# Kernel optimization log

Measured on AMD Instinct MI355X. Metric: run time of the kernel, lower is better.

## Reference

```python
import jax, jax.numpy as jnp
import numpy as np

E = 16        # num_experts
TOPK = 2      # num_experts_per_tok


def setup_inputs() -> dict:
    key = jax.random.key(0)
    ks = jax.random.split(key, 8)
    B, S, H, I, IS = 4, 2048, 1024, 512, 2048
    std = 0.02
    return {
        "hidden_states": jax.random.normal(ks[0], (B, S, H), jnp.float32),
        "gate_w": jax.random.normal(ks[1], (E, H), jnp.float32) * std,
        "gate_up_proj": jax.random.normal(ks[2], (E, 2 * I, H), jnp.float32) * std,
        "down_proj": jax.random.normal(ks[3], (E, H, I), jnp.float32) * std,
        "shared_gate_proj": jax.random.normal(ks[4], (IS, H), jnp.float32) * std,
        "shared_up_proj": jax.random.normal(ks[5], (IS, H), jnp.float32) * std,
        "shared_down_proj": jax.random.normal(ks[6], (H, IS), jnp.float32) * std,
        "shared_expert_gate_w": jax.random.normal(ks[7], (1, H), jnp.float32) * std,
    }


def _moe(x, gate_w, gate_up_proj, down_proj, sgp, sup, sdp, segw):
    # x: [N, H] flattened tokens
    N = x.shape[0]
    router_logits = x @ gate_w.T                      # [N, E]
    probs = jax.nn.softmax(router_logits, axis=-1)
    routing_weights, selected = jax.lax.top_k(probs, TOPK)   # [N, TOPK]
    routing_weights = routing_weights / routing_weights.sum(-1, keepdims=True)
    # combine weights scattered into dense [N, E] (per-token per-expert gate)
    combine = jnp.zeros((N, E), x.dtype).at[jnp.arange(N)[:, None], selected].add(routing_weights)

    def body(acc, ws):
        gu_w, d_w, cw = ws                            # [2I,H], [H,I], [N]
        gu = x @ gu_w.T                               # [N, 2I]
        g, u = jnp.split(gu, 2, axis=-1)
        h = jax.nn.silu(g) * u                        # [N, I]
        return acc + cw[:, None] * (h @ d_w.T), None

    expert_out, _ = jax.lax.scan(body, jnp.zeros_like(x), (gate_up_proj, down_proj, combine.T))

    # shared expert with sigmoid token gate
    shared_h = jax.nn.silu(x @ sgp.T) * (x @ sup.T)   # [N, IS]
    shared_out = (shared_h @ sdp.T) * jax.nn.sigmoid(x @ segw.T)  # [N, H]
    out = expert_out + shared_out

    # aux (load-balancing) loss
    counts = jnp.sum(jax.nn.one_hot(selected, E, dtype=x.dtype), axis=(0, 1))  # [E]
    frac_tokens = counts / (N * TOPK)
    frac_probs = probs.sum(0) / N
    aux_loss = E * jnp.sum(frac_tokens * frac_probs)
    return out, aux_loss


def reference(hidden_states, gate_w, gate_up_proj, down_proj, shared_gate_proj, shared_up_proj, shared_down_proj, shared_expert_gate_w):
    B, S, H = hidden_states.shape
    out, aux = _moe(hidden_states.reshape(-1, H), gate_w, gate_up_proj, down_proj,
                    shared_gate_proj, shared_up_proj, shared_down_proj, shared_expert_gate_w)
    return out.reshape(B, S, H), aux
```

## Files before the change

kernel.cpp:

```cpp
#include <hip/hip_runtime.h>
#include <hip/hip_bf16.h>
#include <stdint.h>


#define N_TOK 8192
#define HDIM 1024
#define NEXP 16
#define IEXP 512
#define ISH 2048

typedef __bf16 bf16x8 __attribute__((ext_vector_type(8)));
typedef float f32x4 __attribute__((ext_vector_type(4)));

#define OFF_XBF   ((size_t)0)
#define OFF_WSG   ((size_t)16777216)
#define OFF_WSU   ((size_t)20971520)
#define OFF_WSD   ((size_t)25165824)
#define OFF_SH    ((size_t)29360128)
#define OFF_HEXP  ((size_t)62914560)
#define OFF_IDS   ((size_t)79691776)
#define OFF_META  ((size_t)80216064)
#define OFF_SIG   ((size_t)80216320)
#define OFF_LG    ((size_t)80249088)
#define OFF_SLOT  ((size_t)81297664)
#define OFF_TWAB  ((size_t)81363200)

static __device__ __forceinline__ unsigned short f2bf(float f) {
  unsigned int u = __float_as_uint(f);
  u += 0x7fffu + ((u >> 16) & 1u);
  return (unsigned short)(u >> 16);
}
static __device__ __forceinline__ int pack_bf2(float a, float b) {
  return (int)f2bf(a) | ((int)f2bf(b) << 16);
}
static __device__ __forceinline__ float bf2f(unsigned short u) {
  return __uint_as_float(((unsigned int)u) << 16);
}
static __device__ __forceinline__ void gl_lds16(const void* g, void* l) {
  __builtin_amdgcn_global_load_lds(
      (const __attribute__((address_space(1))) unsigned int*)g,
      (__attribute__((address_space(3))) unsigned int*)l, 16, 0, 0);
}

__global__ void cvt_kernel(const float* __restrict__ src,
                           unsigned short* __restrict__ dst, int n4) {
  int i = blockIdx.x * 256 + threadIdx.x;
  if (i >= n4) return;
  float4 v = ((const float4*)src)[i];
  uint2 o;
  o.x = (unsigned)pack_bf2(v.x, v.y);
  o.y = (unsigned)pack_bf2(v.z, v.w);
  ((uint2*)dst)[i] = o;
}

__global__ __launch_bounds__(256) void logits_kernel(
    const float* __restrict__ X, const float* __restrict__ GW,
    const float* __restrict__ SEGW, float* __restrict__ LG,
    unsigned short* __restrict__ XBF) {
  int wid = threadIdx.x >> 6, lane = threadIdx.x & 63;
  int tok = blockIdx.x * 4 + wid;
  const float* xr = X + (size_t)tok * HDIM;
  unsigned short* xw = XBF + (size_t)tok * HDIM;
  float xv[16];
#pragma unroll
  for (int i = 0; i < 16; i++) xv[i] = xr[lane + 64 * i];
#pragma unroll
  for (int i = 0; i < 16; i++) xw[lane + 64 * i] = f2bf(xv[i]);
  float myv = 0.f;
#pragma unroll
  for (int e = 0; e < 17; e++) {
    const float* wr = (e < 16) ? (GW + (size_t)e * HDIM) : SEGW;
    float p = 0.f;
#pragma unroll
    for (int i = 0; i < 16; i++) p += xv[i] * wr[lane + 64 * i];
#pragma unroll
    for (int off = 32; off >= 1; off >>= 1) p += __shfl_xor(p, off, 64);
    if (lane == e) myv = p;
  }
  if (lane < 17) LG[(size_t)tok * 32 + lane] = myv;
}

__global__ __launch_bounds__(256) void route_kernel(
    const float* __restrict__ LG, int* __restrict__ cnt,
    float* __restrict__ pps, int* __restrict__ ids,
    int* __restrict__ slotAB, float* __restrict__ twAB,
    float* __restrict__ sig) {
  __shared__ int lcnt[16];
  __shared__ int lbase[16];
  __shared__ float lps[16];
  int tid = threadIdx.x;
  int tok = blockIdx.x * 256 + tid;
  if (tid < 16) { lcnt[tid] = 0; lps[tid] = 0.f; }
  __syncthreads();
  const float4* row = (const float4*)(LG + (size_t)tok * 32);
  float4 v0 = row[0], v1 = row[1], v2 = row[2], v3 = row[3];
  float g16 = row[4].x;
  float lg[16] = {v0.x, v0.y, v0.z, v0.w, v1.x, v1.y, v1.z, v1.w,
                  v2.x, v2.y, v2.z, v2.w, v3.x, v3.y, v3.z, v3.w};
  float mx = lg[0];
#pragma unroll
  for (int e = 1; e < 16; e++) mx = fmaxf(mx, lg[e]);
  float pr[16], s = 0.f;
#pragma unroll
  for (int e = 0; e < 16; e++) { pr[e] = __expf(lg[e] - mx); s += pr[e]; }
  float inv_s = 1.f / s;
  float p1 = -1.f, p2 = -1.f; int i1 = 0, i2 = 0;
#pragma unroll
  for (int e = 0; e < 16; e++) {
    if (pr[e] > p1) { p2 = p1; i2 = i1; p1 = pr[e]; i1 = e; }
    else if (pr[e] > p2) { p2 = pr[e]; i2 = e; }
  }
  float wsum = p1 + p2;
  int s1 = atomicAdd(&lcnt[i1], 1);
  int s2 = atomicAdd(&lcnt[i2], 1);
#pragma unroll
  for (int e = 0; e < 16; e++) atomicAdd(&lps[e], pr[e] * inv_s);
  sig[tok] = 1.f / (1.f + __expf(-g16));
  __syncthreads();
  if (tid < 16) {
    lbase[tid] = atomicAdd(&cnt[tid], lcnt[tid]);
    atomicAdd(&pps[tid], lps[tid]);
  }
  __syncthreads();
  int sl1 = lbase[i1] + s1, sl2 = lbase[i2] + s2;
  ids[i1 * N_TOK + sl1] = tok;
  ids[i2 * N_TOK + sl2] = tok;
  slotAB[tok * 2]     = (i1 << 14) | sl1;
  slotAB[tok * 2 + 1] = (i2 << 14) | sl2;
  twAB[tok * 2]     = p1 / wsum;
  twAB[tok * 2 + 1] = p2 / wsum;
}

__global__ void offs_aux_kernel(const int* __restrict__ cnt, int* __restrict__ off,
                                const float* __restrict__ probs_sum,
                                float* __restrict__ out_aux) {
  if (threadIdx.x == 0 && blockIdx.x == 0) {
    int run = 0; float aux = 0.f;
    for (int e = 0; e < NEXP; e++) {
      off[e] = run; run += cnt[e];
      aux += ((float)cnt[e] / (float)(N_TOK * 2)) * (probs_sum[e] / (float)N_TOK);
    }
    off[16] = run;
    *out_aux = (float)NEXP * aux;
  }
}

__global__ __launch_bounds__(256) void shared_gemm1_kernel(
    const unsigned short* __restrict__ X, const unsigned short* __restrict__ Wg,
    const unsigned short* __restrict__ Wu, unsigned short* __restrict__ H) {
  __shared__ __align__(16) unsigned short As[128 * 32];
  __shared__ __align__(16) unsigned short Bs1[64 * 32];
  __shared__ __align__(16) unsigned short Bs2[64 * 32];
  int m0 = blockIdx.y * 128, n0 = blockIdx.x * 64;
  int t = threadIdx.x, lane = t & 63, w = t >> 6;
  int wm = (w & 1) * 64, wn = (w >> 1) * 32;
  int arow = t >> 2, akb = (t & 3) * 8;
  const unsigned short* ap0 = X + (size_t)(m0 + arow) * HDIM + akb;
  const unsigned short* ap1 = X + (size_t)(m0 + 64 + arow) * HDIM + akb;
  const unsigned short* bp1 = Wg + (size_t)(n0 + arow) * HDIM + akb;
  const unsigned short* bp2 = Wu + (size_t)(n0 + arow) * HDIM + akb;
  f32x4 z = {0.f, 0.f, 0.f, 0.f};
  f32x4 accg[4][2], accu[4][2];
#pragma unroll
  for (int i = 0; i < 4; i++)
#pragma unroll
    for (int j = 0; j < 2; j++) { accg[i][j] = z; accu[i][j] = z; }
  for (int k0 = 0; k0 < HDIM; k0 += 32) {
    __syncthreads();
    gl_lds16(ap0 + k0, &As[t * 8]);
    gl_lds16(ap1 + k0, &As[2048 + t * 8]);
    gl_lds16(bp1 + k0, &Bs1[t * 8]);
    gl_lds16(bp2 + k0, &Bs2[t * 8]);
    __syncthreads();
    int fr = lane & 15, fc = (lane >> 4) * 8;
    bf16x8 af[4], bg[2], bu[2];
#pragma unroll
    for (int i = 0; i < 4; i++) af[i] = *(const bf16x8*)&As[(wm + i * 16 + fr) * 32 + fc];
#pragma unroll
    for (int j = 0; j < 2; j++) {
      bg[j] = *(const bf16x8*)&Bs1[(wn + j * 16 + fr) * 32 + fc];
      bu[j] = *(const bf16x8*)&Bs2[(wn + j * 16 + fr) * 32 + fc];
    }
#pragma unroll
    for (int i = 0; i < 4; i++)
#pragma unroll
      for (int j = 0; j < 2; j++) {
        accg[i][j] = __builtin_amdgcn_mfma_f32_16x16x32_bf16(af[i], bg[j], accg[i][j], 0, 0, 0);
        accu[i][j] = __builtin_amdgcn_mfma_f32_16x16x32_bf16(af[i], bu[j], accu[i][j], 0, 0, 0);
      }
  }
  int col = lane & 15, rq = (lane >> 4) * 4;
#pragma unroll
  for (int i = 0; i < 4; i++)
#pragma unroll
    for (int j = 0; j < 2; j++)
#pragma unroll
      for (int r = 0; r < 4; r++) {
        int mm = m0 + wm + i * 16 + rq + r;
        int nn = n0 + wn + j * 16 + col;
        float g = accg[i][j][r], u = accu[i][j][r];
        float h = g / (1.f + __expf(-g)) * u;
        H[(size_t)mm * ISH + nn] = f2bf(h);
      }
}

__global__ __launch_bounds__(256) void shared_gemm2_kernel(
    const unsigned short* __restrict__ H, const unsigned short* __restrict__ Wd,
    const float* __restrict__ sig, float* __restrict__ Out) {
  __shared__ __align__(16) unsigned short As[128 * 32];
  __shared__ __align__(16) unsigned short Bs[128 * 32];
  int m0 = blockIdx.y * 128, n0 = blockIdx.x * 128;
  int t = threadIdx.x, lane = t & 63, w = t >> 6;
  int wm = (w & 1) * 64, wn = (w >> 1) * 64;
  int arow = t >> 2, akb = (t & 3) * 8;
  const unsigned short* apA0 = H + (size_t)(m0 + arow) * ISH + akb;
  const unsigned short* apA1 = H + (size_t)(m0 + 64 + arow) * ISH + akb;
  const unsigned short* apB0 = Wd + (size_t)(n0 + arow) * ISH + akb;
  const unsigned short* apB1 = Wd + (size_t)(n0 + 64 + arow) * ISH + akb;
  f32x4 z = {0.f, 0.f, 0.f, 0.f};
  f32x4 acc[4][4];
#pragma unroll
  for (int i = 0; i < 4; i++)
#pragma unroll
    for (int j = 0; j < 4; j++) acc[i][j] = z;
  for (int k0 = 0; k0 < ISH; k0 += 32) {
    __syncthreads();
    gl_lds16(apA0 + k0, &As[t * 8]);
    gl_lds16(apA1 + k0, &As[2048 + t * 8]);
    gl_lds16(apB0 + k0, &Bs[t * 8]);
    gl_lds16(apB1 + k0, &Bs[2048 + t * 8]);
    __syncthreads();
    int fr = lane & 15, fc = (lane >> 4) * 8;
    bf16x8 af[4], bfr[4];
#pragma unroll
    for (int i = 0; i < 4; i++) {
      af[i] = *(const bf16x8*)&As[(wm + i * 16 + fr) * 32 + fc];
      bfr[i] = *(const bf16x8*)&Bs[(wn + i * 16 + fr) * 32 + fc];
    }
#pragma unroll
    for (int i = 0; i < 4; i++)
#pragma unroll
      for (int j = 0; j < 4; j++)
        acc[i][j] = __builtin_amdgcn_mfma_f32_16x16x32_bf16(af[i], bfr[j], acc[i][j], 0, 0, 0);
  }
  int col = lane & 15, rq = (lane >> 4) * 4;
#pragma unroll
  for (int i = 0; i < 4; i++)
#pragma unroll
    for (int r = 0; r < 4; r++) {
      int mm = m0 + wm + i * 16 + rq + r;
      float sg = sig[mm];
#pragma unroll
      for (int j = 0; j < 4; j++) {
        int nn = n0 + wn + j * 16 + col;
        Out[(size_t)mm * HDIM + nn] = acc[i][j][r] * sg;
      }
    }
}

__global__ __launch_bounds__(256) void exp_gemm1_kernel(
    const unsigned short* __restrict__ X, const unsigned short* __restrict__ WGUb,
    const int* __restrict__ ids, const int* __restrict__ cnt,
    const int* __restrict__ off, unsigned short* __restrict__ Hexp) {
  int e = blockIdx.z;
  int ne = cnt[e];
  int m0 = blockIdx.y * 128;
  if (m0 >= ne) return;
  __shared__ __align__(16) unsigned short As[128 * 32];
  __shared__ __align__(16) unsigned short Bs1[64 * 32];
  __shared__ __align__(16) unsigned short Bs2[64 * 32];
  int n0 = blockIdx.x * 64;
  const int* eids = ids + e * N_TOK;
  int base = off[e];
  int t = threadIdx.x, lane = t & 63, w = t >> 6;
  int wm = (w & 1) * 64, wn = (w >> 1) * 32;
  int arow = t >> 2, akb = (t & 3) * 8;
  int s0 = m0 + arow, s1 = m0 + 64 + arow;
  int t0 = (s0 < ne) ? eids[s0] : 0;
  int t1 = (s1 < ne) ? eids[s1] : 0;
  const unsigned short* ap0 = X + (size_t)t0 * HDIM + akb;
  const unsigned short* ap1 = X + (size_t)t1 * HDIM + akb;
  const unsigned short* bpg = WGUb + ((size_t)e * 1024 + n0 + arow) * HDIM + akb;
  const unsigned short* bpu = WGUb + ((size_t)e * 1024 + 512 + n0 + arow) * HDIM + akb;
  f32x4 z = {0.f, 0.f, 0.f, 0.f};
  f32x4 accg[4][2], accu[4][2];
#pragma unroll
  for (int i = 0; i < 4; i++)
#pragma unroll
    for (int j = 0; j < 2; j++) { accg[i][j] = z; accu[i][j] = z; }
  for (int k0 = 0; k0 < HDIM; k0 += 32) {
    __syncthreads();
    gl_lds16(ap0 + k0, &As[t * 8]);
    gl_lds16(ap1 + k0, &As[2048 + t * 8]);
    gl_lds16(bpg + k0, &Bs1[t * 8]);
    gl_lds16(bpu + k0, &Bs2[t * 8]);
    __syncthreads();
    int fr = lane & 15, fc = (lane >> 4) * 8;
    bf16x8 af[4], bg[2], bu[2];
#pragma unroll
    for (int i = 0; i < 4; i++) af[i] = *(const bf16x8*)&As[(wm + i * 16 + fr) * 32 + fc];
#pragma unroll
    for (int j = 0; j < 2; j++) {
      bg[j] = *(const bf16x8*)&Bs1[(wn + j * 16 + fr) * 32 + fc];
      bu[j] = *(const bf16x8*)&Bs2[(wn + j * 16 + fr) * 32 + fc];
    }
#pragma unroll
    for (int i = 0; i < 4; i++)
#pragma unroll
      for (int j = 0; j < 2; j++) {
        accg[i][j] = __builtin_amdgcn_mfma_f32_16x16x32_bf16(af[i], bg[j], accg[i][j], 0, 0, 0);
        accu[i][j] = __builtin_amdgcn_mfma_f32_16x16x32_bf16(af[i], bu[j], accu[i][j], 0, 0, 0);
      }
  }
  int col = lane & 15, rq = (lane >> 4) * 4;
#pragma unroll
  for (int i = 0; i < 4; i++)
#pragma unroll
    for (int j = 0; j < 2; j++)
#pragma unroll
      for (int r = 0; r < 4; r++) {
        int slot = m0 + wm + i * 16 + rq + r;
        if (slot < ne) {
          int nn = n0 + wn + j * 16 + col;
          float g = accg[i][j][r], u = accu[i][j][r];
          float h = g / (1.f + __expf(-g)) * u;
          Hexp[(size_t)(base + slot) * IEXP + nn] = f2bf(h);
        }
      }
}

__global__ __launch_bounds__(256) void exp_gemm2_kernel(
    const unsigned short* __restrict__ Hexp, const unsigned short* __restrict__ WDb,
    const int* __restrict__ cnt, const int* __restrict__ off,
    unsigned short* __restrict__ Eout) {
  int e = blockIdx.z;
  int ne = cnt[e];
  int m0 = blockIdx.y * 128;
  if (m0 >= ne) return;
  __shared__ __align__(16) unsigned short As[128 * 32];
  __shared__ __align__(16) unsigned short Bs[128 * 32];
  int n0 = blockIdx.x * 128;
  int base = off[e];
  int t = threadIdx.x, lane = t & 63, w = t >> 6;
  int wm = (w & 1) * 64, wn = (w >> 1) * 64;
  int arow = t >> 2, akb = (t & 3) * 8;
  int ra0 = base + m0 + arow;        if (ra0 > 16383) ra0 = 16383;
  int ra1 = base + m0 + 64 + arow;   if (ra1 > 16383) ra1 = 16383;
  const unsigned short* ap0 = Hexp + (size_t)ra0 * IEXP + akb;
  const unsigned short* ap1 = Hexp + (size_t)ra1 * IEXP + akb;
  const unsigned short* bp0 = WDb + ((size_t)e * HDIM + n0 + arow) * IEXP + akb;
  const unsigned short* bp1 = WDb + ((size_t)e * HDIM + n0 + 64 + arow) * IEXP + akb;
  f32x4 z = {0.f, 0.f, 0.f, 0.f};
  f32x4 acc[4][4];
#pragma unroll
  for (int i = 0; i < 4; i++)
#pragma unroll
    for (int j = 0; j < 4; j++) acc[i][j] = z;
  for (int k0 = 0; k0 < IEXP; k0 += 32) {
    __syncthreads();
    gl_lds16(ap0 + k0, &As[t * 8]);
    gl_lds16(ap1 + k0, &As[2048 + t * 8]);
    gl_lds16(bp0 + k0, &Bs[t * 8]);
    gl_lds16(bp1 + k0, &Bs[2048 + t * 8]);
    __syncthreads();
    int fr = lane & 15, fc = (lane >> 4) * 8;
    bf16x8 af[4], bfr[4];
#pragma unroll
    for (int i = 0; i < 4; i++) {
      af[i] = *(const bf16x8*)&As[(wm + i * 16 + fr) * 32 + fc];
      bfr[i] = *(const bf16x8*)&Bs[(wn + i * 16 + fr) * 32 + fc];
    }
#pragma unroll
    for (int i = 0; i < 4; i++)
#pragma unroll
      for (int j = 0; j < 4; j++)
        acc[i][j] = __builtin_amdgcn_mfma_f32_16x16x32_bf16(af[i], bfr[j], acc[i][j], 0, 0, 0);
  }
  int col = lane & 15, rq = (lane >> 4) * 4;
#pragma unroll
  for (int i = 0; i < 4; i++)
#pragma unroll
    for (int r = 0; r < 4; r++) {
      int slot = m0 + wm + i * 16 + rq + r;
      if (slot < ne) {
#pragma unroll
        for (int j = 0; j < 4; j++) {
          int nn = n0 + wn + j * 16 + col;
          Eout[(size_t)(base + slot) * HDIM + nn] = f2bf(acc[i][j][r]);
        }
      }
    }
}

__global__ __launch_bounds__(256) void combine_kernel(
    const unsigned short* __restrict__ Eout, const int* __restrict__ slotAB,
    const float* __restrict__ twAB, const int* __restrict__ off,
    float* __restrict__ Out) {
  int tok = blockIdx.x, t = threadIdx.x;
  int sa = slotAB[tok * 2], sb = slotAB[tok * 2 + 1];
  float wa = twAB[tok * 2], wb = twAB[tok * 2 + 1];
  int ra = off[sa >> 14] + (sa & 16383);
  int rb = off[sb >> 14] + (sb & 16383);
  const ushort4 a4 = *(const ushort4*)(Eout + (size_t)ra * HDIM + t * 4);
  const ushort4 b4 = *(const ushort4*)(Eout + (size_t)rb * HDIM + t * 4);
  float* po = Out + (size_t)tok * HDIM + t * 4;
  float4 o = *(const float4*)po;
  o.x += wa * bf2f(a4.x) + wb * bf2f(b4.x);
  o.y += wa * bf2f(a4.y) + wb * bf2f(b4.y);
  o.z += wa * bf2f(a4.z) + wb * bf2f(b4.z);
  o.w += wa * bf2f(a4.w) + wb * bf2f(b4.w);
  *(float4*)po = o;
}

extern "C" void kernel_launch(void* const* d_in, const int* in_sizes, int n_in,
                              void* d_out, int out_size, void* d_ws, size_t ws_size,
                              hipStream_t stream) {
  const float* X   = (const float*)d_in[0];
  const float* GW  = (const float*)d_in[1];
  const float* WGU = (const float*)d_in[2];
  const float* WDN = (const float*)d_in[3];
  const float* WSG = (const float*)d_in[4];
  const float* WSU = (const float*)d_in[5];
  const float* WSD = (const float*)d_in[6];
  const float* SEGW = (const float*)d_in[7];
  float* Out = (float*)d_out;
  char* ws = (char*)d_ws;

  unsigned short* xbf  = (unsigned short*)(ws + OFF_XBF);
  unsigned short* wsg  = (unsigned short*)(ws + OFF_WSG);
  unsigned short* wsu  = (unsigned short*)(ws + OFF_WSU);
  unsigned short* wsd  = (unsigned short*)(ws + OFF_WSD);
  unsigned short* sh   = (unsigned short*)(ws + OFF_SH);
  unsigned short* hexp = (unsigned short*)(ws + OFF_HEXP);
  int*   ids  = (int*)(ws + OFF_IDS);
  int*   cnt  = (int*)(ws + OFF_META);
  int*   off  = (int*)(ws + OFF_META + 64);
  float* pps  = (float*)(ws + OFF_META + 144);
  float* sig  = (float*)(ws + OFF_SIG);
  float* lg   = (float*)(ws + OFF_LG);
  int*   slotAB = (int*)(ws + OFF_SLOT);
  float* twAB   = (float*)(ws + OFF_TWAB);
  unsigned short* wgu_bf = (unsigned short*)(ws + OFF_SH);
  unsigned short* wdn_bf = (unsigned short*)(ws + OFF_XBF);
  unsigned short* eout   = (unsigned short*)(ws + OFF_SH);

  hipMemsetAsync(ws + OFF_META, 0, 256, stream);

  {
    int n4;
    n4 = (ISH * HDIM) / 4;
    cvt_kernel<<<(n4 + 255) / 256, 256, 0, stream>>>(WSG, wsg, n4);
    cvt_kernel<<<(n4 + 255) / 256, 256, 0, stream>>>(WSU, wsu, n4);
    n4 = (HDIM * ISH) / 4;
    cvt_kernel<<<(n4 + 255) / 256, 256, 0, stream>>>(WSD, wsd, n4);
  }

  logits_kernel<<<N_TOK / 4, 256, 0, stream>>>(X, GW, SEGW, lg, xbf);
  route_kernel<<<N_TOK / 256, 256, 0, stream>>>(lg, cnt, pps, ids, slotAB, twAB, sig);
  offs_aux_kernel<<<1, 64, 0, stream>>>(cnt, off, pps, Out + (size_t)N_TOK * HDIM);

  shared_gemm1_kernel<<<dim3(ISH / 64, N_TOK / 128), 256, 0, stream>>>(xbf, wsg, wsu, sh);
  shared_gemm2_kernel<<<dim3(HDIM / 128, N_TOK / 128), 256, 0, stream>>>(sh, wsd, sig, Out);

  {
    int n4 = (NEXP * 2 * IEXP * HDIM) / 4;
    cvt_kernel<<<(n4 + 255) / 256, 256, 0, stream>>>(WGU, wgu_bf, n4);
  }
  exp_gemm1_kernel<<<dim3(IEXP / 64, N_TOK / 128, NEXP), 256, 0, stream>>>(
      xbf, wgu_bf, ids, cnt, off, hexp);
  {
    int n4 = (NEXP * HDIM * IEXP) / 4;
    cvt_kernel<<<(n4 + 255) / 256, 256, 0, stream>>>(WDN, wdn_bf, n4);
  }
  exp_gemm2_kernel<<<dim3(HDIM / 128, N_TOK / 128, NEXP), 256, 0, stream>>>(
      hexp, wdn_bf, cnt, off, eout);
  combine_kernel<<<N_TOK, 256, 0, stream>>>(eout, slotAB, twAB, off, Out);
}
```

Measured before the change: 491.5 us.

## Use BK=64 XOR-swizzled LDS tiles and batch weight conversions into one launch

All four GEMM kernels now stage K-tiles of 64 instead of 32 into LDS, with an XOR swizzle on the column offset. This halves the number of barrier pairs per K loop and is meant to avoid LDS bank conflicts on the fragment reads. shared_gemm2 moves to 64-wide N tiles, which doubles its grid. When the workspace is large enough, the five weight fp32-to-bf16 conversions are fused into a single cvt5 launch into separate buffers, removing four launches. The larger LDS footprint per block may lower occupancy.

```diff
diff --git a/kernel.cpp b/kernel.cpp
--- a/kernel.cpp
+++ b/kernel.cpp
@@ -24,6 +24,9 @@
 #define OFF_LG    ((size_t)80249088)
 #define OFF_SLOT  ((size_t)81297664)
 #define OFF_TWAB  ((size_t)81363200)
+#define OFF_WGU2  ((size_t)81428736)
+#define OFF_WDN2  ((size_t)114983168)
+#define WS_NEED_ROOMY ((size_t)131760384)
 
 static __device__ __forceinline__ unsigned short f2bf(float f) {
   unsigned int u = __float_as_uint(f);
@@ -51,6 +54,30 @@
   o.x = (unsigned)pack_bf2(v.x, v.y);
   o.y = (unsigned)pack_bf2(v.z, v.w);
   ((uint2*)dst)[i] = o;
+}
+
+__global__ void cvt5_kernel(const float* s0, unsigned short* d0, int c0,
+                            const float* s1, unsigned short* d1, int c1,
+                            const float* s2, unsigned short* d2, int c2,
+                            const float* s3, unsigned short* d3, int c3,
+                            const float* s4, unsigned short* d4, int c4) {
+  int i = blockIdx.x * 256 + threadIdx.x;
+  const float* s; unsigned short* d;
+  if (i < c0) { s = s0; d = d0; }
+  else { i -= c0;
+  if (i < c1) { s = s1; d = d1; }
+  else { i -= c1;
+  if (i < c2) { s = s2; d = d2; }
+  else { i -= c2;
+  if (i < c3) { s = s3; d = d3; }
+  else { i -= c3;
+  if (i < c4) { s = s4; d = d4; }
+  else return; }}}}
+  float4 v = ((const float4*)s)[i];
+  uint2 o;
+  o.x = (unsigned)pack_bf2(v.x, v.y);
+  o.y = (unsigned)pack_bf2(v.z, v.w);
+  ((uint2*)d)[i] = o;
 }
 
 __global__ __launch_bounds__(256) void logits_kernel(
@@ -145,49 +172,65 @@
   }
 }
 
+
 __global__ __launch_bounds__(256) void shared_gemm1_kernel(
     const unsigned short* __restrict__ X, const unsigned short* __restrict__ Wg,
     const unsigned short* __restrict__ Wu, unsigned short* __restrict__ H) {
-  __shared__ __align__(16) unsigned short As[128 * 32];
-  __shared__ __align__(16) unsigned short Bs1[64 * 32];
-  __shared__ __align__(16) unsigned short Bs2[64 * 32];
+  __shared__ __align__(16) unsigned short As[128 * 64];
+  __shared__ __align__(16) unsigned short Bs1[64 * 64];
+  __shared__ __align__(16) unsigned short Bs2[64 * 64];
   int m0 = blockIdx.y * 128, n0 = blockIdx.x * 64;
   int t = threadIdx.x, lane = t & 63, w = t >> 6;
   int wm = (w & 1) * 64, wn = (w >> 1) * 32;
-  int arow = t >> 2, akb = (t & 3) * 8;
-  const unsigned short* ap0 = X + (size_t)(m0 + arow) * HDIM + akb;
-  const unsigned short* ap1 = X + (size_t)(m0 + 64 + arow) * HDIM + akb;
-  const unsigned short* bp1 = Wg + (size_t)(n0 + arow) * HDIM + akb;
-  const unsigned short* bp2 = Wu + (size_t)(n0 + arow) * HDIM + akb;
+  int srow = t >> 3;
+  int scol = (((t & 7) ^ (srow & 7)) * 8);
+  const unsigned short* apA[4];
+#pragma unroll
+  for (int r = 0; r < 4; r++) apA[r] = X + (size_t)(m0 + r * 32 + srow) * HDIM + scol;
+  const unsigned short* apB1[2];
+  const unsigned short* apB2[2];
+#pragma unroll
+  for (int r = 0; r < 2; r++) {
+    apB1[r] = Wg + (size_t)(n0 + r * 32 + srow) * HDIM + scol;
+    apB2[r] = Wu + (size_t)(n0 + r * 32 + srow) * HDIM + scol;
+  }
+  int fr = lane & 15, q = lane >> 4, sw = fr & 7;
+  int fo0 = ((q ^ sw) * 8), fo1 = (((4 + q) ^ sw) * 8);
   f32x4 z = {0.f, 0.f, 0.f, 0.f};
   f32x4 accg[4][2], accu[4][2];
 #pragma unroll
   for (int i = 0; i < 4; i++)
 #pragma unroll
     for (int j = 0; j < 2; j++) { accg[i][j] = z; accu[i][j] = z; }
-  for (int k0 = 0; k0 < HDIM; k0 += 32) {
-    __syncthreads();
-    gl_lds16(ap0 + k0, &As[t * 8]);
-    gl_lds16(ap1 + k0, &As[2048 + t * 8]);
-    gl_lds16(bp1 + k0, &Bs1[t * 8]);
-    gl_lds16(bp2 + k0, &Bs2[t * 8]);
-    __syncthreads();
-    int fr = lane & 15, fc = (lane >> 4) * 8;
-    bf16x8 af[4], bg[2], bu[2];
-#pragma unroll
-    for (int i = 0; i < 4; i++) af[i] = *(const bf16x8*)&As[(wm + i * 16 + fr) * 32 + fc];
-#pragma unroll
-    for (int j = 0; j < 2; j++) {
-      bg[j] = *(const bf16x8*)&Bs1[(wn + j * 16 + fr) * 32 + fc];
-      bu[j] = *(const bf16x8*)&Bs2[(wn + j * 16 + fr) * 32 + fc];
-    }
-#pragma unroll
-    for (int i = 0; i < 4; i++)
+  for (int k0 = 0; k0 < HDIM; k0 += 64) {
+    __syncthreads();
+#pragma unroll
+    for (int r = 0; r < 4; r++) gl_lds16(apA[r] + k0, &As[r * 2048 + t * 8]);
+#pragma unroll
+    for (int r = 0; r < 2; r++) {
+      gl_lds16(apB1[r] + k0, &Bs1[r * 2048 + t * 8]);
+      gl_lds16(apB2[r] + k0, &Bs2[r * 2048 + t * 8]);
+    }
+    __syncthreads();
+#pragma unroll
+    for (int kk = 0; kk < 2; kk++) {
+      int fo = kk ? fo1 : fo0;
+      bf16x8 af[4], bg[2], bu[2];
+#pragma unroll
+      for (int i = 0; i < 4; i++) af[i] = *(const bf16x8*)&As[(wm + i * 16 + fr) * 64 + fo];
 #pragma unroll
       for (int j = 0; j < 2; j++) {
-        accg[i][j] = __builtin_amdgcn_mfma_f32_16x16x32_bf16(af[i], bg[j], accg[i][j], 0, 0, 0);
-        accu[i][j] = __builtin_amdgcn_mfma_f32_16x16x32_bf16(af[i], bu[j], accu[i][j], 0, 0, 0);
-      }
+        bg[j] = *(const bf16x8*)&Bs1[(wn + j * 16 + fr) * 64 + fo];
+        bu[j] = *(const bf16x8*)&Bs2[(wn + j * 16 + fr) * 64 + fo];
+      }
+#pragma unroll
+      for (int i = 0; i < 4; i++)
+#pragma unroll
+        for (int j = 0; j < 2; j++) {
+          accg[i][j] = __builtin_amdgcn_mfma_f32_16x16x32_bf16(af[i], bg[j], accg[i][j], 0, 0, 0);
+          accu[i][j] = __builtin_amdgcn_mfma_f32_16x16x32_bf16(af[i], bu[j], accu[i][j], 0, 0, 0);
+        }
+    }
   }
   int col = lane & 15, rq = (lane >> 4) * 4;
 #pragma unroll
@@ -207,41 +250,48 @@
 __global__ __launch_bounds__(256) void shared_gemm2_kernel(
     const unsigned short* __restrict__ H, const unsigned short* __restrict__ Wd,
     const float* __restrict__ sig, float* __restrict__ Out) {
-  __shared__ __align__(16) unsigned short As[128 * 32];
-  __shared__ __align__(16) unsigned short Bs[128 * 32];
-  int m0 = blockIdx.y * 128, n0 = blockIdx.x * 128;
+  __shared__ __align__(16) unsigned short As[128 * 64];
+  __shared__ __align__(16) unsigned short Bs[64 * 64];
+  int m0 = blockIdx.y * 128, n0 = blockIdx.x * 64;
   int t = threadIdx.x, lane = t & 63, w = t >> 6;
-  int wm = (w & 1) * 64, wn = (w >> 1) * 64;
-  int arow = t >> 2, akb = (t & 3) * 8;
-  const unsigned short* apA0 = H + (size_t)(m0 + arow) * ISH + akb;
-  const unsigned short* apA1 = H + (size_t)(m0 + 64 + arow) * ISH + akb;
-  const unsigned short* apB0 = Wd + (size_t)(n0 + arow) * ISH + akb;
-  const unsigned short* apB1 = Wd + (size_t)(n0 + 64 + arow) * ISH + akb;
+  int wm = (w & 1) * 64, wn = (w >> 1) * 32;
+  int srow = t >> 3;
+  int scol = (((t & 7) ^ (srow & 7)) * 8);
+  const unsigned short* apA[4];
+#pragma unroll
+  for (int r = 0; r < 4; r++) apA[r] = H + (size_t)(m0 + r * 32 + srow) * ISH + scol;
+  const unsigned short* apB[2];
+#pragma unroll
+  for (int r = 0; r < 2; r++) apB[r] = Wd + (size_t)(n0 + r * 32 + srow) * ISH + scol;
+  int fr = lane & 15, q = lane >> 4, sw = fr & 7;
+  int fo0 = ((q ^ sw) * 8), fo1 = (((4 + q) ^ sw) * 8);
   f32x4 z = {0.f, 0.f, 0.f, 0.f};
-  f32x4 acc[4][4];
-#pragma unroll
-  for (int i = 0; i < 4; i++)
-#pragma unroll
-    for (int j = 0; j < 4; j++) acc[i][j] = z;
-  for (int k0 = 0; k0 < ISH; k0 += 32) {
-    __syncthreads();
-    gl_lds16(apA0 + k0, &As[t * 8]);
-    gl_lds16(apA1 + k0, &As[2048 + t * 8]);
-    gl_lds16(apB0 + k0, &Bs[t * 8]);
-    gl_lds16(apB1 + k0, &Bs[2048 + t * 8]);
-    __syncthreads();
-    int fr = lane & 15, fc = (lane >> 4) * 8;
-    bf16x8 af[4], bfr[4];
-#pragma unroll
-    for (int i = 0; i < 4; i++) {
-      af[i] = *(const bf16x8*)&As[(wm + i * 16 + fr) * 32 + fc];
-      bfr[i] = *(const bf16x8*)&Bs[(wn + i * 16 + fr) * 32 + fc];
-    }
-#pragma unroll
-    for (int i = 0; i < 4; i++)
-#pragma unroll
-      for (int j = 0; j < 4; j++)
-        acc[i][j] = __builtin_amdgcn_mfma_f32_16x16x32_bf16(af[i], bfr[j], acc[i][j], 0, 0, 0);
+  f32x4 acc[4][2];
+#pragma unroll
+  for (int i = 0; i < 4; i++)
+#pragma unroll
+    for (int j = 0; j < 2; j++) acc[i][j] = z;
+  for (int k0 = 0; k0 < ISH; k0 += 64) {
+    __syncthreads();
+#pragma unroll
+    for (int r = 0; r < 4; r++) gl_lds16(apA[r] + k0, &As[r * 2048 + t * 8]);
+#pragma unroll
+    for (int r = 0; r < 2; r++) gl_lds16(apB[r] + k0, &Bs[r * 2048 + t * 8]);
+    __syncthreads();
+#pragma unroll
+    for (int kk = 0; kk < 2; kk++) {
+      int fo = kk ? fo1 : fo0;
+      bf16x8 af[4], bfr[2];
+#pragma unroll
+      for (int i = 0; i < 4; i++) af[i] = *(const bf16x8*)&As[(wm + i * 16 + fr) * 64 + fo];
+#pragma unroll
+      for (int j = 0; j < 2; j++) bfr[j] = *(const bf16x8*)&Bs[(wn + j * 16 + fr) * 64 + fo];
+#pragma unroll
+      for (int i = 0; i < 4; i++)
+#pragma unroll
+        for (int j = 0; j < 2; j++)
+          acc[i][j] = __builtin_amdgcn_mfma_f32_16x16x32_bf16(af[i], bfr[j], acc[i][j], 0, 0, 0);
+    }
   }
   int col = lane & 15, rq = (lane >> 4) * 4;
 #pragma unroll
@@ -251,7 +301,7 @@
       int mm = m0 + wm + i * 16 + rq + r;
       float sg = sig[mm];
 #pragma unroll
-      for (int j = 0; j < 4; j++) {
+      for (int j = 0; j < 2; j++) {
         int nn = n0 + wn + j * 16 + col;
         Out[(size_t)mm * HDIM + nn] = acc[i][j][r] * sg;
       }
@@ -266,51 +316,67 @@
   int ne = cnt[e];
   int m0 = blockIdx.y * 128;
   if (m0 >= ne) return;
-  __shared__ __align__(16) unsigned short As[128 * 32];
-  __shared__ __align__(16) unsigned short Bs1[64 * 32];
-  __shared__ __align__(16) unsigned short Bs2[64 * 32];
+  __shared__ __align__(16) unsigned short As[128 * 64];
+  __shared__ __align__(16) unsigned short Bs1[64 * 64];
+  __shared__ __align__(16) unsigned short Bs2[64 * 64];
   int n0 = blockIdx.x * 64;
   const int* eids = ids + e * N_TOK;
   int base = off[e];
   int t = threadIdx.x, lane = t & 63, w = t >> 6;
   int wm = (w & 1) * 64, wn = (w >> 1) * 32;
-  int arow = t >> 2, akb = (t & 3) * 8;
-  int s0 = m0 + arow, s1 = m0 + 64 + arow;
-  int t0 = (s0 < ne) ? eids[s0] : 0;
-  int t1 = (s1 < ne) ? eids[s1] : 0;
-  const unsigned short* ap0 = X + (size_t)t0 * HDIM + akb;
-  const unsigned short* ap1 = X + (size_t)t1 * HDIM + akb;
-  const unsigned short* bpg = WGUb + ((size_t)e * 1024 + n0 + arow) * HDIM + akb;
-  const unsigned short* bpu = WGUb + ((size_t)e * 1024 + 512 + n0 + arow) * HDIM + akb;
+  int srow = t >> 3;
+  int scol = (((t & 7) ^ (srow & 7)) * 8);
+  const unsigned short* apA[4];
+#pragma unroll
+  for (int r = 0; r < 4; r++) {
+    int slot = m0 + r * 32 + srow;
+    int tok = (slot < ne) ? eids[slot] : 0;
+    apA[r] = X + (size_t)tok * HDIM + scol;
+  }
+  const unsigned short* apB1[2];
+  const unsigned short* apB2[2];
+#pragma unroll
+  for (int r = 0; r < 2; r++) {
+    apB1[r] = WGUb + ((size_t)e * 1024 + n0 + r * 32 + srow) * HDIM + scol;
+    apB2[r] = WGUb + ((size_t)e * 1024 + 512 + n0 + r * 32 + srow) * HDIM + scol;
+  }
+  int fr = lane & 15, q = lane >> 4, sw = fr & 7;
+  int fo0 = ((q ^ sw) * 8), fo1 = (((4 + q) ^ sw) * 8);
   f32x4 z = {0.f, 0.f, 0.f, 0.f};
   f32x4 accg[4][2], accu[4][2];
 #pragma unroll
   for (int i = 0; i < 4; i++)
 #pragma unroll
     for (int j = 0; j < 2; j++) { accg[i][j] = z; accu[i][j] = z; }
-  for (int k0 = 0; k0 < HDIM; k0 += 32) {
-    __syncthreads();
-    gl_lds16(ap0 + k0, &As[t * 8]);
-    gl_lds16(ap1 + k0, &As[2048 + t * 8]);
-    gl_lds16(bpg + k0, &Bs1[t * 8]);
-    gl_lds16(bpu + k0, &Bs2[t * 8]);
-    __syncthreads();
-    int fr = lane & 15, fc = (lane >> 4) * 8;
-    bf16x8 af[4], bg[2], bu[2];
-#pragma unroll
-    for (int i = 0; i < 4; i++) af[i] = *(const bf16x8*)&As[(wm + i * 16 + fr) * 32 + fc];
-#pragma unroll
-    for (int j = 0; j < 2; j++) {
-      bg[j] = *(const bf16x8*)&Bs1[(wn + j * 16 + fr) * 32 + fc];
-      bu[j] = *(const bf16x8*)&Bs2[(wn + j * 16 + fr) * 32 + fc];
-    }
-#pragma unroll
-    for (int i = 0; i < 4; i++)
+  for (int k0 = 0; k0 < HDIM; k0 += 64) {
+    __syncthreads();
+#pragma unroll
+    for (int r = 0; r < 4; r++) gl_lds16(apA[r] + k0, &As[r * 2048 + t * 8]);
+#pragma unroll
+    for (int r = 0; r < 2; r++) {
+      gl_lds16(apB1[r] + k0, &Bs1[r * 2048 + t * 8]);
+      gl_lds16(apB2[r] + k0, &Bs2[r * 2048 + t * 8]);
+    }
+    __syncthreads();
+#pragma unroll
+    for (int kk = 0; kk < 2; kk++) {
+      int fo = kk ? fo1 : fo0;
+      bf16x8 af[4], bg[2], bu[2];
+#pragma unroll
+      for (int i = 0; i < 4; i++) af[i] = *(const bf16x8*)&As[(wm + i * 16 + fr) * 64 + fo];
 #pragma unroll
       for (int j = 0; j < 2; j++) {
-        accg[i][j] = __builtin_amdgcn_mfma_f32_16x16x32_bf16(af[i], bg[j], accg[i][j], 0, 0, 0);
-        accu[i][j] = __builtin_amdgcn_mfma_f32_16x16x32_bf16(af[i], bu[j], accu[i][j], 0, 0, 0);
-      }
+        bg[j] = *(const bf16x8*)&Bs1[(wn + j * 16 + fr) * 64 + fo];
+        bu[j] = *(const bf16x8*)&Bs2[(wn + j * 16 + fr) * 64 + fo];
+      }
+#pragma unroll
+      for (int i = 0; i < 4; i++)
+#pragma unroll
+        for (int j = 0; j < 2; j++) {
+          accg[i][j] = __builtin_amdgcn_mfma_f32_16x16x32_bf16(af[i], bg[j], accg[i][j], 0, 0, 0);
+          accu[i][j] = __builtin_amdgcn_mfma_f32_16x16x32_bf16(af[i], bu[j], accu[i][j], 0, 0, 0);
+        }
+    }
   }
   int col = lane & 15, rq = (lane >> 4) * 4;
 #pragma unroll
@@ -337,44 +403,56 @@
   int ne = cnt[e];
   int m0 = blockIdx.y * 128;
   if (m0 >= ne) return;
-  __shared__ __align__(16) unsigned short As[128 * 32];
-  __shared__ __align__(16) unsigned short Bs[128 * 32];
+  __shared__ __align__(16) unsigned short As[128 * 64];
+  __shared__ __align__(16) unsigned short Bs[128 * 64];
   int n0 = blockIdx.x * 128;
   int base = off[e];
   int t = threadIdx.x, lane = t & 63, w = t >> 6;
   int wm = (w & 1) * 64, wn = (w >> 1) * 64;
-  int arow = t >> 2, akb = (t & 3) * 8;
-  int ra0 = base + m0 + arow;        if (ra0 > 16383) ra0 = 16383;
-  int ra1 = base + m0 + 64 + arow;   if (ra1 > 16383) ra1 = 16383;
-  const unsigned short* ap0 = Hexp + (size_t)ra0 * IEXP + akb;
-  const unsigned short* ap1 = Hexp + (size_t)ra1 * IEXP + akb;
-  const unsigned short* bp0 = WDb + ((size_t)e * HDIM + n0 + arow) * IEXP + akb;
-  const unsigned short* bp1 = WDb + ((size_t)e * HDIM + n0 + 64 + arow) * IEXP + akb;
+  int srow = t >> 3;
+  int scol = (((t & 7) ^ (srow & 7)) * 8);
+  const unsigned short* apA[4];
+#pragma unroll
+  for (int r = 0; r < 4; r++) {
+    int ra = base + m0 + r * 32 + srow;
+    if (ra > 16383) ra = 16383;
+    apA[r] = Hexp + (size_t)ra * IEXP + scol;
+  }
+  const unsigned short* apB[4];
+#pragma unroll
+  for (int r = 0; r < 4; r++)
+    apB[r] = WDb + ((size_t)e * HDIM + n0 + r * 32 + srow) * IEXP + scol;
+  int fr = lane & 15, q = lane >> 4, sw = fr & 7;
+  int fo0 = ((q ^ sw) * 8), fo1 = (((4 + q) ^ sw) * 8);
   f32x4 z = {0.f, 0.f, 0.f, 0.f};
   f32x4 acc[4][4];
 #pragma unroll
   for (int i = 0; i < 4; i++)
 #pragma unroll
     for (int j = 0; j < 4; j++) acc[i][j] = z;
-  for (int k0 = 0; k0 < IEXP; k0 += 32) {
-    __syncthreads();
-    gl_lds16(ap0 + k0, &As[t * 8]);
-    gl_lds16(ap1 + k0, &As[2048 + t * 8]);
-    gl_lds16(bp0 + k0, &Bs[t * 8]);
-    gl_lds16(bp1 + k0, &Bs[2048 + t * 8]);
-    __syncthreads();
-    int fr = lane & 15, fc = (lane >> 4) * 8;
-    bf16x8 af[4], bfr[4];
-#pragma unroll
-    for (int i = 0; i < 4; i++) {
-      af[i] = *(const bf16x8*)&As[(wm + i * 16 + fr) * 32 + fc];
-      bfr[i] = *(const bf16x8*)&Bs[(wn + i * 16 + fr) * 32 + fc];
-    }
-#pragma unroll
-    for (int i = 0; i < 4; i++)
-#pragma unroll
-      for (int j = 0; j < 4; j++)
-        acc[i][j] = __builtin_amdgcn_mfma_f32_16x16x32_bf16(af[i], bfr[j], acc[i][j], 0, 0, 0);
+  for (int k0 = 0; k0 < IEXP; k0 += 64) {
+    __syncthreads();
+#pragma unroll
+    for (int r = 0; r < 4; r++) {
+      gl_lds16(apA[r] + k0, &As[r * 2048 + t * 8]);
+      gl_lds16(apB[r] + k0, &Bs[r * 2048 + t * 8]);
+    }
+    __syncthreads();
+#pragma unroll
+    for (int kk = 0; kk < 2; kk++) {
+      int fo = kk ? fo1 : fo0;
+      bf16x8 af[4], bfr[4];
+#pragma unroll
+      for (int i = 0; i < 4; i++) {
+        af[i] = *(const bf16x8*)&As[(wm + i * 16 + fr) * 64 + fo];
+        bfr[i] = *(const bf16x8*)&Bs[(wn + i * 16 + fr) * 64 + fo];
+      }
+#pragma unroll
+      for (int i = 0; i < 4; i++)
+#pragma unroll
+        for (int j = 0; j < 4; j++)
+          acc[i][j] = __builtin_amdgcn_mfma_f32_16x16x32_bf16(af[i], bfr[j], acc[i][j], 0, 0, 0);
+    }
   }
   int col = lane & 15, rq = (lane >> 4) * 4;
 #pragma unroll
@@ -440,19 +518,26 @@
   float* lg   = (float*)(ws + OFF_LG);
   int*   slotAB = (int*)(ws + OFF_SLOT);
   float* twAB   = (float*)(ws + OFF_TWAB);
-  unsigned short* wgu_bf = (unsigned short*)(ws + OFF_SH);
-  unsigned short* wdn_bf = (unsigned short*)(ws + OFF_XBF);
-  unsigned short* eout   = (unsigned short*)(ws + OFF_SH);
+  unsigned short* eout = (unsigned short*)(ws + OFF_SH);
+
+  const bool roomy = (ws_size >= WS_NEED_ROOMY);
+  unsigned short* wgu_bf = (unsigned short*)(ws + (roomy ? OFF_WGU2 : OFF_SH));
+  unsigned short* wdn_bf = (unsigned short*)(ws + (roomy ? OFF_WDN2 : OFF_XBF));
 
   hipMemsetAsync(ws + OFF_META, 0, 256, stream);
 
-  {
-    int n4;
-    n4 = (ISH * HDIM) / 4;
-    cvt_kernel<<<(n4 + 255) / 256, 256, 0, stream>>>(WSG, wsg, n4);
-    cvt_kernel<<<(n4 + 255) / 256, 256, 0, stream>>>(WSU, wsu, n4);
-    n4 = (HDIM * ISH) / 4;
-    cvt_kernel<<<(n4 + 255) / 256, 256, 0, stream>>>(WSD, wsd, n4);
+  const int c_wsg = (ISH * HDIM) / 4, c_wsd = (HDIM * ISH) / 4;
+  const int c_wgu = (NEXP * 2 * IEXP * HDIM) / 4, c_wdn = (NEXP * HDIM * IEXP) / 4;
+  if (roomy) {
+    int tot = c_wsg * 2 + c_wsd + c_wgu + c_wdn;
+    cvt5_kernel<<<(tot + 255) / 256, 256, 0, stream>>>(
+        WSG, wsg, c_wsg, WSU, wsu, c_wsg, WSD, wsd, c_wsd,
+        WGU, wgu_bf, c_wgu, WDN, wdn_bf, c_wdn);
+  } else {
+    int tot = c_wsg * 2 + c_wsd;
+    cvt5_kernel<<<(tot + 255) / 256, 256, 0, stream>>>(
+        WSG, wsg, c_wsg, WSU, wsu, c_wsg, WSD, wsd, c_wsd,
+        (const float*)0, (unsigned short*)0, 0, (const float*)0, (unsigned short*)0, 0);
   }
 
   logits_kernel<<<N_TOK / 4, 256, 0, stream>>>(X, GW, SEGW, lg, xbf);
@@ -460,18 +545,14 @@
   offs_aux_kernel<<<1, 64, 0, stream>>>(cnt, off, pps, Out + (size_t)N_TOK * HDIM);
 
   shared_gemm1_kernel<<<dim3(ISH / 64, N_TOK / 128), 256, 0, stream>>>(xbf, wsg, wsu, sh);
-  shared_gemm2_kernel<<<dim3(HDIM / 128, N_TOK / 128), 256, 0, stream>>>(sh, wsd, sig, Out);
-
-  {
-    int n4 = (NEXP * 2 * IEXP * HDIM) / 4;
-    cvt_kernel<<<(n4 + 255) / 256, 256, 0, stream>>>(WGU, wgu_bf, n4);
-  }
+  shared_gemm2_kernel<<<dim3(HDIM / 64, N_TOK / 128), 256, 0, stream>>>(sh, wsd, sig, Out);
+
+  if (!roomy)
+    cvt_kernel<<<(c_wgu + 255) / 256, 256, 0, stream>>>(WGU, wgu_bf, c_wgu);
   exp_gemm1_kernel<<<dim3(IEXP / 64, N_TOK / 128, NEXP), 256, 0, stream>>>(
       xbf, wgu_bf, ids, cnt, off, hexp);
-  {
-    int n4 = (NEXP * HDIM * IEXP) / 4;
-    cvt_kernel<<<(n4 + 255) / 256, 256, 0, stream>>>(WDN, wdn_bf, n4);
-  }
+  if (!roomy)
+    cvt_kernel<<<(c_wdn + 255) / 256, 256, 0, stream>>>(WDN, wdn_bf, c_wdn);
   exp_gemm2_kernel<<<dim3(HDIM / 128, N_TOK / 128, NEXP), 256, 0, stream>>>(
       hexp, wdn_bf, cnt, off, eout);
   combine_kernel<<<N_TOK, 256, 0, stream>>>(eout, slotAB, twAB, off, Out);
```

After: 498.8 us. Within noise of the previous version (+1.5%).
